# Kernel optimization log

Measured on AMD Instinct MI355X. Metric: run time of the kernel, lower is better.

## Reference

```python
import jax, jax.numpy as jnp
import numpy as np

N_NODES = 500_000
N_EDGES = 32_000_000

def setup_inputs() -> dict:
    key = jax.random.key(0)
    k1, k2, k3 = jax.random.split(key, 3)
    x = jax.random.uniform(k1, (N_NODES, 1), dtype=jnp.float32)
    edge_index = jax.random.randint(k2, (2, N_EDGES), 0, N_NODES, dtype=jnp.int32)
    edge_probs = jax.random.uniform(k3, (N_EDGES,), dtype=jnp.float32)
    edge_weight = jnp.ones((1,), dtype=jnp.float32)
    self_loop = jnp.ones((1,), dtype=jnp.float32)
    return {"x": x, "edge_index": edge_index, "edge_probs": edge_probs,
            "edge_weight": edge_weight, "self_loop": self_loop}

def reference(x, edge_index, edge_probs, edge_weight, self_loop):
    # x: (N,1), edge_index: (2,E), edge_probs: (E,)
    src = edge_index[0]
    dst = edge_index[1]
    # messages: (E,1) = 1 - x[src] * p_e * w
    messages = 1.0 - x[src] * edge_probs[:, None] * edge_weight
    # scatter-multiply into dst nodes; nodes with no incoming edges get 1
    agg = jax.ops.segment_prod(messages, dst, num_segments=x.shape[0])
    return agg + self_loop * x
```

## Files before the change

kernel.cpp:

```cpp
#include <hip/hip_runtime.h>


#if defined(__has_builtin) && __has_builtin(__builtin_amdgcn_exp2f)
#define EXP2F(v) __builtin_amdgcn_exp2f(v)
#else
#define EXP2F(v) exp2f(v)
#endif

#define BLK 256
#define NB_SHIFT 13
#define NB (1 << NB_SHIFT)
#define EPB 4096
#define MAXK 256

__device__ __forceinline__ unsigned xcc_id() {
    return __builtin_amdgcn_s_getreg((31 << 11) | 20) & 7u;
}
__device__ __forceinline__ void atomic_fadd_l2(float* p, float v) {
    asm volatile("global_atomic_add_f32 %0, %1, off" :: "v"(p), "v"(v) : "memory");
}
__device__ __forceinline__ void atomic_fadd_agent(float* p, float v) {
    unsafeAtomicAdd(p, v);
}

__global__ void init_zero(float* __restrict__ ws, int n) {
    int i = blockIdx.x * blockDim.x + threadIdx.x;
    if (i < n) ws[i] = 0.0f;
}

template <bool USE_L2>
__global__ __launch_bounds__(256) void edge_scatter(
        const float* __restrict__ x,
        const int* __restrict__ src,
        const int* __restrict__ dst,
        const float* __restrict__ probs,
        const float* __restrict__ w_ptr,
        float* __restrict__ logsum,
        int n_nodes, int n_e4) {
    const float w = w_ptr[0];
    float* ls = USE_L2 ? (logsum + (size_t)xcc_id() * (size_t)n_nodes) : logsum;
    int i = blockIdx.x * blockDim.x + threadIdx.x;
    if (i >= n_e4) return;
    int4   s = ((const int4*)src)[i];
    int4   d = ((const int4*)dst)[i];
    float4 p = ((const float4*)probs)[i];
    float m0 = __log2f(1.0f - x[s.x] * p.x * w);
    float m1 = __log2f(1.0f - x[s.y] * p.y * w);
    float m2 = __log2f(1.0f - x[s.z] * p.z * w);
    float m3 = __log2f(1.0f - x[s.w] * p.w * w);
    if (USE_L2) {
        atomic_fadd_l2(&ls[d.x], m0); atomic_fadd_l2(&ls[d.y], m1);
        atomic_fadd_l2(&ls[d.z], m2); atomic_fadd_l2(&ls[d.w], m3);
    } else {
        atomic_fadd_agent(&ls[d.x], m0); atomic_fadd_agent(&ls[d.y], m1);
        atomic_fadd_agent(&ls[d.z], m2); atomic_fadd_agent(&ls[d.w], m3);
    }
}

template <bool USE_L2>
__global__ void edge_scatter_tail(
        const float* __restrict__ x,
        const int* __restrict__ src,
        const int* __restrict__ dst,
        const float* __restrict__ probs,
        const float* __restrict__ w_ptr,
        float* __restrict__ logsum,
        int n_nodes, int start, int n_edges) {
    const float w = w_ptr[0];
    float* ls = USE_L2 ? (logsum + (size_t)xcc_id() * (size_t)n_nodes) : logsum;
    int i = start + blockIdx.x * blockDim.x + threadIdx.x;
    if (i >= n_edges) return;
    float m = __log2f(1.0f - x[src[i]] * probs[i] * w);
    if (USE_L2) atomic_fadd_l2(&ls[dst[i]], m);
    else        atomic_fadd_agent(&ls[dst[i]], m);
}

__global__ void finalize8(const float* __restrict__ x,
                          const float* __restrict__ sl_ptr,
                          const float* __restrict__ logsum,
                          float* __restrict__ out, int n) {
    int i = blockIdx.x * blockDim.x + threadIdx.x;
    if (i >= n) return;
    float s = 0.0f;
    #pragma unroll
    for (int r = 0; r < 8; ++r) s += logsum[(size_t)r * n + i];
    out[i] = EXP2F(s) + sl_ptr[0] * x[i];
}

__global__ void finalize1(const float* __restrict__ x,
                          const float* __restrict__ sl_ptr,
                          const float* __restrict__ logsum,
                          float* __restrict__ out, int n) {
    int i = blockIdx.x * blockDim.x + threadIdx.x;
    if (i < n) out[i] = EXP2F(logsum[i]) + sl_ptr[0] * x[i];
}


__global__ __launch_bounds__(256) void k_hist(
        const int* __restrict__ dstp,
        unsigned* __restrict__ hist,
        int ebase, int ecount, int K, int G0, int vec_ok) {
    __shared__ unsigned h[MAXK];
    const int b = blockIdx.x;
    const int t = threadIdx.x;
    for (int i = t; i < K; i += BLK) h[i] = 0;
    __syncthreads();
    const int begin = ebase + b * EPB;
    const int end   = min(begin + EPB, ebase + ecount);
    if (vec_ok) {
        for (int e0 = begin + t * 4; e0 < end; e0 += BLK * 4) {
            if (e0 + 4 <= end) {
                const int4 d = *(const int4*)(dstp + e0);
                atomicAdd(&h[(unsigned)d.x >> NB_SHIFT], 1u);
                atomicAdd(&h[(unsigned)d.y >> NB_SHIFT], 1u);
                atomicAdd(&h[(unsigned)d.z >> NB_SHIFT], 1u);
                atomicAdd(&h[(unsigned)d.w >> NB_SHIFT], 1u);
            } else {
                for (int e = e0; e < end; ++e)
                    atomicAdd(&h[(unsigned)dstp[e] >> NB_SHIFT], 1u);
            }
        }
    } else {
        for (int e0 = begin + t * 4; e0 < end; e0 += BLK * 4) {
            const int ee = min(e0 + 4, end);
            for (int e = e0; e < ee; ++e)
                atomicAdd(&h[(unsigned)dstp[e] >> NB_SHIFT], 1u);
        }
    }
    __syncthreads();
    for (int i = t; i < K; i += BLK) hist[(size_t)i * G0 + b] = h[i];
}

__global__ __launch_bounds__(256) void k_scan_row(
        unsigned* __restrict__ hist, unsigned* __restrict__ btot,
        int G0, int Gr) {
    __shared__ unsigned wsum[4];
    __shared__ unsigned carry;
    const int k = blockIdx.x;
    const int t = threadIdx.x;
    unsigned* row = hist + (size_t)k * G0;
    if (t == 0) carry = 0;
    __syncthreads();
    for (int c0 = 0; c0 < Gr; c0 += BLK) {
        const unsigned v = (c0 + t < Gr) ? row[c0 + t] : 0u;
        unsigned xs = v;
        #pragma unroll
        for (int o = 1; o < 64; o <<= 1) {
            const unsigned y = __shfl_up(xs, o, 64);
            if ((t & 63) >= o) xs += y;
        }
        if ((t & 63) == 63) wsum[t >> 6] = xs;
        __syncthreads();
        unsigned woff = 0;
        for (int wv = 0; wv < (t >> 6); ++wv) woff += wsum[wv];
        const unsigned ex = xs + woff - v + carry;
        if (c0 + t < Gr) row[c0 + t] = ex;
        const unsigned ctot = wsum[0] + wsum[1] + wsum[2] + wsum[3];
        __syncthreads();
        if (t == 0) carry += ctot;
        __syncthreads();
    }
    if (t == 0) btot[k] = carry;
}

__global__ __launch_bounds__(256) void k_scan_bkt(
        const unsigned* __restrict__ btot, unsigned* __restrict__ bbase, int K) {
    __shared__ unsigned wsum[4];
    const int t = threadIdx.x;
    const unsigned v = (t < K) ? ((btot[t] + 1u) & ~1u) : 0u;
    unsigned xs = v;
    #pragma unroll
    for (int o = 1; o < 64; o <<= 1) {
        const unsigned y = __shfl_up(xs, o, 64);
        if ((t & 63) >= o) xs += y;
    }
    if ((t & 63) == 63) wsum[t >> 6] = xs;
    __syncthreads();
    unsigned woff = 0;
    for (int wv = 0; wv < (t >> 6); ++wv) woff += wsum[wv];
    if (t < K) bbase[t] = xs + woff - v;
}

__global__ __launch_bounds__(256) void k_scatter(
        const float* __restrict__ x,
        const int* __restrict__ src,
        const int* __restrict__ dstp,
        const float* __restrict__ probs,
        const float* __restrict__ w_ptr,
        const unsigned* __restrict__ base,
        const unsigned* __restrict__ btot,
        const unsigned* __restrict__ bbase,
        uint2* __restrict__ queue,
        int ebase, int ecount, int K, int G0, int Gr, int vec_ok) {
    __shared__ uint2    stage[EPB];
    __shared__ unsigned off_s[MAXK + 1];
    __shared__ unsigned cur_s[MAXK];
    __shared__ unsigned gb2_s[MAXK];
    __shared__ unsigned wsum[4];
    const int b = blockIdx.x;
    const int t = threadIdx.x;
    if (K <= 0) return;

    unsigned v = 0, gbeg = 0;
    if (t < K) {
        const unsigned cme = base[(size_t)t * G0 + b];
        const unsigned cnx = (b + 1 < Gr) ? base[(size_t)t * G0 + b + 1] : btot[t];
        v = cnx - cme;
        gbeg = bbase[t] + cme;
    }
    unsigned xs = v;
    #pragma unroll
    for (int o = 1; o < 64; o <<= 1) {
        const unsigned y = __shfl_up(xs, o, 64);
        if ((t & 63) >= o) xs += y;
    }
    if ((t & 63) == 63) wsum[t >> 6] = xs;
    __syncthreads();
    unsigned woff = 0;
    for (int wv = 0; wv < (t >> 6); ++wv) woff += wsum[wv];
    const unsigned ex = xs + woff - v;
    if (t < K) {
        off_s[t] = ex;
        cur_s[t] = ex;
        gb2_s[t] = gbeg - ex;
    }
    if (t == 0) off_s[K] = wsum[0] + wsum[1] + wsum[2] + wsum[3];
    __syncthreads();

    const float w = w_ptr[0];
    const int begin = ebase + b * EPB;
    const int end   = min(begin + EPB, ebase + ecount);
    auto one = [&](int e) {
        const int dv = dstp[e];
        const float m = __log2f(1.0f - x[src[e]] * probs[e] * w);
        const unsigned kk = (unsigned)dv >> NB_SHIFT;
        const unsigned r = atomicAdd(&cur_s[kk], 1u);
        stage[r] = make_uint2((unsigned)dv & (NB - 1), __float_as_uint(m));
    };
    if (vec_ok) {
        for (int e0 = begin + t * 4; e0 < end; e0 += BLK * 4) {
            if (e0 + 4 <= end) {
                const int4   d  = *(const int4*)(dstp + e0);
                const int4   sv = *(const int4*)(src + e0);
                const float4 pv = *(const float4*)(probs + e0);
                const float m0 = __log2f(1.0f - x[sv.x] * pv.x * w);
                const float m1 = __log2f(1.0f - x[sv.y] * pv.y * w);
                const float m2 = __log2f(1.0f - x[sv.z] * pv.z * w);
                const float m3 = __log2f(1.0f - x[sv.w] * pv.w * w);
                const unsigned r0 = atomicAdd(&cur_s[(unsigned)d.x >> NB_SHIFT], 1u);
                stage[r0] = make_uint2((unsigned)d.x & (NB - 1), __float_as_uint(m0));
                const unsigned r1 = atomicAdd(&cur_s[(unsigned)d.y >> NB_SHIFT], 1u);
                stage[r1] = make_uint2((unsigned)d.y & (NB - 1), __float_as_uint(m1));
                const unsigned r2 = atomicAdd(&cur_s[(unsigned)d.z >> NB_SHIFT], 1u);
                stage[r2] = make_uint2((unsigned)d.z & (NB - 1), __float_as_uint(m2));
                const unsigned r3 = atomicAdd(&cur_s[(unsigned)d.w >> NB_SHIFT], 1u);
                stage[r3] = make_uint2((unsigned)d.w & (NB - 1), __float_as_uint(m3));
            } else {
                for (int e = e0; e < end; ++e) one(e);
            }
        }
    } else {
        for (int e0 = begin + t * 4; e0 < end; e0 += BLK * 4) {
            const int ee = min(e0 + 4, end);
            for (int e = e0; e < ee; ++e) one(e);
        }
    }
    __syncthreads();

    const int total = end - begin;
    for (int j = t; j < total; j += BLK) {
        const uint2 e = stage[j];
        int lo = 0, hi = K;
        while (hi - lo > 1) {
            const int mid = (lo + hi) >> 1;
            if ((unsigned)j >= off_s[mid]) lo = mid; else hi = mid;
        }
        queue[(size_t)gb2_s[lo] + (unsigned)j] = e;
    }
}

__global__ __launch_bounds__(256) void k_accum(
        const uint2* __restrict__ queue,
        const unsigned* __restrict__ btot,
        const unsigned* __restrict__ bbase,
        float* __restrict__ partial,
        int s3, int first) {
    __shared__ float acc[NB];
    const int t = threadIdx.x;
    const int k = blockIdx.x / s3;
    const int s = blockIdx.x % s3;
    for (int i = t; i < NB; i += BLK) acc[i] = 0.0f;
    __syncthreads();
    const unsigned cnt = btot[k];
    unsigned per = (cnt + s3 - 1) / s3;
    per = (per + 1u) & ~1u;
    const unsigned lo = min((unsigned)s * per, cnt);
    const unsigned hi = min(lo + per, cnt);
    const unsigned n = hi - lo;
    const uint2* q = queue + bbase[k] + lo;
    const uint4* q4 = (const uint4*)q;
    const unsigned n4 = n >> 1;
    for (unsigned p = t; p < n4; p += BLK) {
        const uint4 e = q4[p];
        atomicAdd(&acc[e.x], __uint_as_float(e.y));
        atomicAdd(&acc[e.z], __uint_as_float(e.w));
    }
    if ((n & 1u) && t == 0) {
        const uint2 e = q[n - 1];
        atomicAdd(&acc[e.x], __uint_as_float(e.y));
    }
    __syncthreads();
    float* p = partial + (size_t)blockIdx.x * NB;
    if (first) { for (int j = t; j < NB; j += BLK) p[j] = acc[j]; }
    else       { for (int j = t; j < NB; j += BLK) p[j] += acc[j]; }
}

__global__ __launch_bounds__(256) void k_final(
        const float* __restrict__ x,
        const float* __restrict__ sl_ptr,
        const float* __restrict__ partial,
        float* __restrict__ out, int n, int s3) {
    int i = blockIdx.x * blockDim.x + threadIdx.x;
    if (i >= n) return;
    const int k = i >> NB_SHIFT;
    const int l = i & (NB - 1);
    const float* p = partial + ((size_t)k * s3) * NB + l;
    float ssum = 0.0f;
    for (int r = 0; r < s3; ++r) ssum += p[(size_t)r * NB];
    out[i] = EXP2F(ssum) + sl_ptr[0] * x[i];
}


static inline size_t alignup256(size_t v) { return (v + 255) & ~(size_t)255; }

extern "C" void kernel_launch(void* const* d_in, const int* in_sizes, int n_in,
                              void* d_out, int out_size, void* d_ws, size_t ws_size,
                              hipStream_t stream) {
    const float* x          = (const float*)d_in[0];
    const int*   edge_index = (const int*)  d_in[1];
    const float* probs      = (const float*)d_in[2];
    const float* w          = (const float*)d_in[3];
    const float* sl         = (const float*)d_in[4];

    const int n_nodes = in_sizes[0];
    const int n_edges = in_sizes[1] / 2;
    const int* src = edge_index;
    const int* dst = edge_index + n_edges;

    const int K = (n_nodes + NB - 1) >> NB_SHIFT;

    int R = 0, s3 = 0, G0 = 0;
    long long Er = 0;
    size_t off_hist = 0, off_btot = 0, off_bbase = 0, off_queue = 0;
    if (n_nodes > 0 && n_edges > 0 && K >= 1 && K <= MAXK) {
        const int s3cand[5] = {16, 8, 4, 2, 1};
        for (int r = 1; r <= 64 && !R; ++r) {
            long long er = (((long long)n_edges + r - 1) / r + 3) & ~3LL;
            if (er < 4) er = 4;
            int g = (int)((er + EPB - 1) / EPB);
            if (g < 1) g = 1;
            for (int ci = 0; ci < 5; ++ci) {
                const int cs3 = s3cand[ci];
                const size_t pb = (size_t)K * cs3 * NB * sizeof(float);
                const size_t hb = (size_t)K * g * sizeof(unsigned);
                const size_t kb = (size_t)K * sizeof(unsigned);
                const size_t o1 = alignup256(pb);
                const size_t o2 = o1 + alignup256(hb);
                const size_t o3 = o2 + alignup256(kb);
                const size_t o4 = o3 + alignup256(kb);
                const size_t tot = o4 + ((size_t)er + 2 * MAXK) * sizeof(uint2);
                if (tot <= ws_size) {
                    R = r; s3 = cs3; G0 = g; Er = er;
                    off_hist = o1; off_btot = o2; off_bbase = o3; off_queue = o4;
                    break;
                }
            }
        }
    }

    if (R > 0) {
        char* wsb = (char*)d_ws;
        float*    partial_p = (float*)wsb;
        unsigned* hist_p    = (unsigned*)(wsb + off_hist);
        unsigned* btot_p    = (unsigned*)(wsb + off_btot);
        unsigned* bbase_p   = (unsigned*)(wsb + off_bbase);
        uint2*    queue_p   = (uint2*)(wsb + off_queue);

        const int vec_ok = ((n_edges & 3) == 0) ? 1 : 0;
        for (int r = 0; r < R; ++r) {
            const long long eb = (long long)r * Er;
            if (eb >= n_edges) break;
            const long long rem = (long long)n_edges - eb;
            const int ec = (int)(rem < Er ? rem : Er);
            const int g = (ec + EPB - 1) / EPB;
            k_hist<<<g, BLK, 0, stream>>>(dst, hist_p, (int)eb, ec, K, G0, vec_ok);
            k_scan_row<<<K, BLK, 0, stream>>>(hist_p, btot_p, G0, g);
            k_scan_bkt<<<1, BLK, 0, stream>>>(btot_p, bbase_p, K);
            k_scatter<<<g, BLK, 0, stream>>>(
                x, src, dst, probs, w, hist_p, btot_p, bbase_p, queue_p,
                (int)eb, ec, K, G0, g, vec_ok);
            k_accum<<<K * s3, BLK, 0, stream>>>(
                queue_p, btot_p, bbase_p, partial_p, s3, r == 0 ? 1 : 0);
        }
        k_final<<<(n_nodes + 255) / 256, 256, 0, stream>>>(
            x, sl, partial_p, (float*)d_out, n_nodes, s3);
        return;
    }

    float* logsum = (float*)d_ws;
    const bool use_l2 = ws_size >= (size_t)8 * (size_t)n_nodes * sizeof(float);
    const int n_ls = use_l2 ? 8 * n_nodes : n_nodes;

    init_zero<<<(n_ls + 255) / 256, 256, 0, stream>>>(logsum, n_ls);

    const int e4 = n_edges / 4;
    const int tail_start = e4 * 4;
    const int tail = n_edges - tail_start;

    if (use_l2) {
        if (e4 > 0)
            edge_scatter<true><<<(e4 + 255) / 256, 256, 0, stream>>>(
                x, src, dst, probs, w, logsum, n_nodes, e4);
        if (tail > 0)
            edge_scatter_tail<true><<<(tail + 255) / 256, 256, 0, stream>>>(
                x, src, dst, probs, w, logsum, n_nodes, tail_start, n_edges);
        finalize8<<<(n_nodes + 255) / 256, 256, 0, stream>>>(
            x, sl, logsum, (float*)d_out, n_nodes);
    } else {
        if (e4 > 0)
            edge_scatter<false><<<(e4 + 255) / 256, 256, 0, stream>>>(
                x, src, dst, probs, w, logsum, n_nodes, e4);
        if (tail > 0)
            edge_scatter_tail<false><<<(tail + 255) / 256, 256, 0, stream>>>(
                x, src, dst, probs, w, logsum, n_nodes, tail_start, n_edges);
        finalize1<<<(n_nodes + 255) / 256, 256, 0, stream>>>(
            x, sl, logsum, (float*)d_out, n_nodes);
    }
}
```

Before: 861.0 us.

## Halve edges per block, store bucket ids, unroll accumulation, allow more splits

```diff
diff --git a/kernel.cpp b/kernel.cpp
--- a/kernel.cpp
+++ b/kernel.cpp
@@ -10,7 +10,7 @@
 #define BLK 256
 #define NB_SHIFT 13
 #define NB (1 << NB_SHIFT)
-#define EPB 4096
+#define EPB 2048
 #define MAXK 256
 
 __device__ __forceinline__ unsigned xcc_id() {
@@ -192,7 +192,8 @@
         const unsigned* __restrict__ bbase,
         uint2* __restrict__ queue,
         int ebase, int ecount, int K, int G0, int Gr, int vec_ok) {
-    __shared__ uint2    stage[EPB];
+    __shared__ uint2         stage[EPB];
+    __shared__ unsigned char bktof[EPB];
     __shared__ unsigned off_s[MAXK + 1];
     __shared__ unsigned cur_s[MAXK];
     __shared__ unsigned gb2_s[MAXK];
@@ -236,6 +237,7 @@
         const unsigned kk = (unsigned)dv >> NB_SHIFT;
         const unsigned r = atomicAdd(&cur_s[kk], 1u);
         stage[r] = make_uint2((unsigned)dv & (NB - 1), __float_as_uint(m));
+        bktof[r] = (unsigned char)kk;
     };
     if (vec_ok) {
         for (int e0 = begin + t * 4; e0 < end; e0 += BLK * 4) {
@@ -247,14 +249,22 @@
                 const float m1 = __log2f(1.0f - x[sv.y] * pv.y * w);
                 const float m2 = __log2f(1.0f - x[sv.z] * pv.z * w);
                 const float m3 = __log2f(1.0f - x[sv.w] * pv.w * w);
-                const unsigned r0 = atomicAdd(&cur_s[(unsigned)d.x >> NB_SHIFT], 1u);
+                const unsigned k0 = (unsigned)d.x >> NB_SHIFT;
+                const unsigned k1 = (unsigned)d.y >> NB_SHIFT;
+                const unsigned k2 = (unsigned)d.z >> NB_SHIFT;
+                const unsigned k3 = (unsigned)d.w >> NB_SHIFT;
+                const unsigned r0 = atomicAdd(&cur_s[k0], 1u);
                 stage[r0] = make_uint2((unsigned)d.x & (NB - 1), __float_as_uint(m0));
-                const unsigned r1 = atomicAdd(&cur_s[(unsigned)d.y >> NB_SHIFT], 1u);
+                bktof[r0] = (unsigned char)k0;
+                const unsigned r1 = atomicAdd(&cur_s[k1], 1u);
                 stage[r1] = make_uint2((unsigned)d.y & (NB - 1), __float_as_uint(m1));
-                const unsigned r2 = atomicAdd(&cur_s[(unsigned)d.z >> NB_SHIFT], 1u);
+                bktof[r1] = (unsigned char)k1;
+                const unsigned r2 = atomicAdd(&cur_s[k2], 1u);
                 stage[r2] = make_uint2((unsigned)d.z & (NB - 1), __float_as_uint(m2));
-                const unsigned r3 = atomicAdd(&cur_s[(unsigned)d.w >> NB_SHIFT], 1u);
+                bktof[r2] = (unsigned char)k2;
+                const unsigned r3 = atomicAdd(&cur_s[k3], 1u);
                 stage[r3] = make_uint2((unsigned)d.w & (NB - 1), __float_as_uint(m3));
+                bktof[r3] = (unsigned char)k3;
             } else {
                 for (int e = e0; e < end; ++e) one(e);
             }
@@ -270,12 +280,8 @@
     const int total = end - begin;
     for (int j = t; j < total; j += BLK) {
         const uint2 e = stage[j];
-        int lo = 0, hi = K;
-        while (hi - lo > 1) {
-            const int mid = (lo + hi) >> 1;
-            if ((unsigned)j >= off_s[mid]) lo = mid; else hi = mid;
-        }
-        queue[(size_t)gb2_s[lo] + (unsigned)j] = e;
+        const unsigned k = bktof[j];
+        queue[(size_t)gb2_s[k] + (unsigned)j] = e;
     }
 }
 
@@ -300,19 +306,28 @@
     const uint2* q = queue + bbase[k] + lo;
     const uint4* q4 = (const uint4*)q;
     const unsigned n4 = n >> 1;
-    for (unsigned p = t; p < n4; p += BLK) {
-        const uint4 e = q4[p];
-        atomicAdd(&acc[e.x], __uint_as_float(e.y));
-        atomicAdd(&acc[e.z], __uint_as_float(e.w));
+    unsigned p = t;
+    for (; p + BLK < n4; p += 2 * BLK) {
+        const uint4 a  = q4[p];
+        const uint4 b2 = q4[p + BLK];
+        atomicAdd(&acc[a.x],  __uint_as_float(a.y));
+        atomicAdd(&acc[a.z],  __uint_as_float(a.w));
+        atomicAdd(&acc[b2.x], __uint_as_float(b2.y));
+        atomicAdd(&acc[b2.z], __uint_as_float(b2.w));
+    }
+    for (; p < n4; p += BLK) {
+        const uint4 a = q4[p];
+        atomicAdd(&acc[a.x], __uint_as_float(a.y));
+        atomicAdd(&acc[a.z], __uint_as_float(a.w));
     }
     if ((n & 1u) && t == 0) {
         const uint2 e = q[n - 1];
         atomicAdd(&acc[e.x], __uint_as_float(e.y));
     }
     __syncthreads();
-    float* p = partial + (size_t)blockIdx.x * NB;
-    if (first) { for (int j = t; j < NB; j += BLK) p[j] = acc[j]; }
-    else       { for (int j = t; j < NB; j += BLK) p[j] += acc[j]; }
+    float* pp = partial + (size_t)blockIdx.x * NB;
+    if (first) { for (int j = t; j < NB; j += BLK) pp[j] = acc[j]; }
+    else       { for (int j = t; j < NB; j += BLK) pp[j] += acc[j]; }
 }
 
 __global__ __launch_bounds__(256) void k_final(
@@ -353,13 +368,13 @@
     long long Er = 0;
     size_t off_hist = 0, off_btot = 0, off_bbase = 0, off_queue = 0;
     if (n_nodes > 0 && n_edges > 0 && K >= 1 && K <= MAXK) {
-        const int s3cand[5] = {16, 8, 4, 2, 1};
+        const int s3cand[6] = {32, 16, 8, 4, 2, 1};
         for (int r = 1; r <= 64 && !R; ++r) {
             long long er = (((long long)n_edges + r - 1) / r + 3) & ~3LL;
             if (er < 4) er = 4;
             int g = (int)((er + EPB - 1) / EPB);
             if (g < 1) g = 1;
-            for (int ci = 0; ci < 5; ++ci) {
+            for (int ci = 0; ci < 6; ++ci) {
                 const int cs3 = s3cand[ci];
                 const size_t pb = (size_t)K * cs3 * NB * sizeof(float);
                 const size_t hb = (size_t)K * g * sizeof(unsigned);
```

After: 902.8 us. +4.9%, slower.
